# Optimization experiments

Measured on AMD Instinct MI355X. Metric: run time of the kernel, lower is better.

Reference implementation:

```python
import jax, jax.numpy as jnp
import numpy as np

SEQ, B, H, NP, HN = 2048, 2, 2048, 16, 128
SCALE = 1.0 / 11.313708498984761  # 1/sqrt(128), hardcoded in the source baddbmm


def setup_inputs() -> dict:
    key = jax.random.key(0)
    k1, k2, k3 = jax.random.split(key, 3)
    return {
        "hidden_states": jax.random.normal(k1, (SEQ, B, H), dtype=jnp.float32),
        "w_qkv": jax.random.normal(k2, (3 * H, H), dtype=jnp.float32) * 0.02,
        "w_out": jax.random.normal(k3, (H, H), dtype=jnp.float32) * 0.02,
    }


def reference(hidden_states, w_qkv, w_out):
    s, b, h = hidden_states.shape
    # QKV projection (column-parallel linear, no bias): [s, b, 3h]
    qkv = hidden_states @ w_qkv.T
    # [s, b, np, 3*hn] then split (num_query_groups == num_heads)
    qkv = qkv.reshape(s, b, NP, 3 * HN)
    q, k, v = qkv[..., :HN], qkv[..., HN:2 * HN], qkv[..., 2 * HN:]
    # baddbmm QK^T with alpha = 1/sqrt(128): scores [b, np, sq, sk]
    scores = jnp.einsum("sbnh,tbnh->bnst", q, k) * SCALE
    # scale_t == 1 then plain softmax (fallback path; no mask applied)
    prob = jax.nn.softmax(scores, axis=-1)
    # context: bmm(prob, V) -> [sq, b, np, hn] -> [sq, b, h]
    ctx = jnp.einsum("bnst,tbnh->sbnh", prob, v).reshape(s, b, h)
    # row-parallel output linear (no bias)
    return ctx @ w_out.T
```

## Files before the change

kernel.cpp:

```cpp
#include <hip/hip_runtime.h>
#include <stdint.h>

#define SEQ 2048
#define BATCH 2
#define HID 2048
#define NHEADS 16
#define HDIM 128
#define QKV_LD 6144
#define SCALE_F 0.08838834764831845f
#define LOG2E_F 1.4426950408889634f

typedef unsigned short u16;
using bf16x8 = __attribute__((ext_vector_type(8))) short;
using f32x4  = __attribute__((ext_vector_type(4))) float;

__device__ inline u16 f2bf(float f) {
  union { float f; uint32_t u; } c; c.f = f;
  uint32_t u = c.u;
  uint32_t r = (u + 0x7fffu + ((u >> 16) & 1u)) >> 16;
  return (u16)r;
}

__device__ inline void gl_lds16(const u16* g, u16* l) {
  __builtin_amdgcn_global_load_lds((const __attribute__((address_space(1))) void*)g,
                                   (__attribute__((address_space(3))) void*)l,
                                   16, 0, 0);
}

__global__ void cvt_all(const float* __restrict__ hs, const float* __restrict__ wqkv,
                        const float* __restrict__ wout, u16* __restrict__ ws_out) {
  int i = blockIdx.x * blockDim.x + threadIdx.x;
  const float* src;
  int j;
  float sc = 1.0f;
  if (i < 2097152) { src = hs; j = i; }
  else if (i < 5242880) {
    j = i - 2097152; src = wqkv;
    const int f = j >> 9;
    if ((f % 384) < 128) sc = SCALE_F;
  } else { j = i - 5242880; src = wout; }
  float4 v = ((const float4*)src)[j];
  ushort4 o;
  o.x = f2bf(v.x * sc); o.y = f2bf(v.y * sc); o.z = f2bf(v.z * sc); o.w = f2bf(v.w * sc);
  ((ushort4*)ws_out)[i] = o;
}

template<bool OUT_BF16>
__global__ __launch_bounds__(256)
void gemm_bt(const u16* __restrict__ A, const u16* __restrict__ Bw,
             void* __restrict__ Cout, int M, int N, int K) {
  __shared__ __align__(16) u16 As[128 * 64];
  __shared__ __align__(16) u16 Bs[128 * 64];
  const int bm = blockIdx.x, bn = blockIdx.y;
  const int tid = threadIdx.x;
  const int wave = tid >> 6, lane = tid & 63;
  const int quad = lane >> 4, l16 = lane & 15;
  const int wm = (wave >> 1) * 64, wn = (wave & 1) * 64;
  f32x4 acc[4][4] = {};

  const u16* Ablk = A + (size_t)(bm * 128) * K;
  const u16* Bblk = Bw + (size_t)(bn * 128) * K;

  for (int k0 = 0; k0 < K; k0 += 64) {
    __syncthreads();
    #pragma unroll
    for (int p = 0; p < 4; ++p) {
      int j = p * 256 + tid;
      int r = j >> 3, cs = j & 7, c = cs ^ (r & 7);
      gl_lds16(Ablk + (size_t)r * K + k0 + c * 8, As + (p * 256 + wave * 64) * 8);
      gl_lds16(Bblk + (size_t)r * K + k0 + c * 8, Bs + (p * 256 + wave * 64) * 8);
    }
    __syncthreads();
    #pragma unroll
    for (int ks = 0; ks < 2; ++ks) {
      bf16x8 af[4], bfr[4];
      #pragma unroll
      for (int mt = 0; mt < 4; ++mt) {
        int row = wm + mt * 16 + l16;
        int cc = (ks * 4 + quad) ^ (row & 7);
        af[mt] = *(const bf16x8*)&As[(row * 8 + cc) * 8];
      }
      #pragma unroll
      for (int nt = 0; nt < 4; ++nt) {
        int row = wn + nt * 16 + l16;
        int cc = (ks * 4 + quad) ^ (row & 7);
        bfr[nt] = *(const bf16x8*)&Bs[(row * 8 + cc) * 8];
      }
      #pragma unroll
      for (int mt = 0; mt < 4; ++mt)
        #pragma unroll
        for (int nt = 0; nt < 4; ++nt)
          acc[mt][nt] = __builtin_amdgcn_mfma_f32_16x16x32_bf16(af[mt], bfr[nt], acc[mt][nt], 0, 0, 0);
    }
  }

  #pragma unroll
  for (int mt = 0; mt < 4; ++mt) {
    #pragma unroll
    for (int nt = 0; nt < 4; ++nt) {
      #pragma unroll
      for (int r = 0; r < 4; ++r) {
        int row = bm * 128 + wm + mt * 16 + quad * 4 + r;
        int col = bn * 128 + wn + nt * 16 + l16;
        float v = acc[mt][nt][r];
        if (OUT_BF16) ((u16*)Cout)[(size_t)row * N + col] = f2bf(v);
        else          ((float*)Cout)[(size_t)row * N + col] = v;
      }
    }
  }
}

__global__ __launch_bounds__(256)
void transpose_v(const u16* __restrict__ qkv, u16* __restrict__ vt) {
  __shared__ u16 Vs[64][132];
  const int st = blockIdx.x, head = blockIdx.y, b = blockIdx.z;
  const int s0 = st * 64;
  const int t = threadIdx.x;
  {
    const int r = t >> 2, c0 = (t & 3) * 32;
    const u16* src = qkv + ((size_t)(s0 + r) * BATCH + b) * QKV_LD + head * 384 + 256 + c0;
    #pragma unroll
    for (int j = 0; j < 4; ++j)
      *(uint4*)&Vs[r][c0 + j * 8] = *(const uint4*)(src + j * 8);
  }
  __syncthreads();
  {
    const int hd = t & 127, sc = (t >> 7) * 32;
    u16 tmp[32];
    #pragma unroll
    for (int j = 0; j < 32; ++j) tmp[j] = Vs[sc + j][hd];
    u16* dst = vt + ((size_t)(b * NHEADS + head) * HDIM + hd) * SEQ + s0 + sc;
    #pragma unroll
    for (int j = 0; j < 4; ++j)
      *(uint4*)&dst[j * 8] = *(const uint4*)&tmp[j * 8];
  }
}

__global__ __launch_bounds__(512, 2)
void attn(const u16* __restrict__ qkv, const u16* __restrict__ vt_g, u16* __restrict__ ctx) {
  const int qt = blockIdx.x, head = blockIdx.y, b = blockIdx.z;
  const int q0 = qt * 256;
  __shared__ __align__(16) u16 Ks[64 * 128];
  __shared__ __align__(16) u16 Vt[144 * 64];
  __shared__ __align__(16) u16 Ps[256 * 72];
  const int tid = threadIdx.x;
  const int wave = tid >> 6, lane = tid & 63;
  const int quad = lane >> 4, l16 = lane & 15;

  const u16* qkv_bh = qkv + (size_t)b * QKV_LD + head * 384;
  const u16* vt = vt_g + (size_t)(b * NHEADS + head) * HDIM * SEQ;

  if (tid < 128) {
    const int row = 128 + (tid >> 3), c = tid & 7;
    const u16 v = (row == 128) ? (u16)0x3F80 : (u16)0;
    ushort4 q4; q4.x = v; q4.y = v; q4.z = v; q4.w = v;
    *(ushort4*)&Vt[(row * 8 + c) * 8] = q4;
    *(ushort4*)&Vt[(row * 8 + c) * 8 + 4] = q4;
  }

  bf16x8 qf[2][4];
  #pragma unroll
  for (int h = 0; h < 4; ++h) {
    __syncthreads();
    #pragma unroll
    for (int p = 0; p < 2; ++p) {
      int j = p * 512 + tid;
      int r = j >> 4, cs = j & 15, c = cs ^ (r & 7);
      gl_lds16(qkv_bh + (size_t)(q0 + h * 64 + r) * (BATCH * QKV_LD) + c * 8,
               Ks + (p * 512 + wave * 64) * 8);
    }
    __syncthreads();
    if ((wave >> 1) == h) {
      #pragma unroll
      for (int mt = 0; mt < 2; ++mt)
        #pragma unroll
        for (int ks = 0; ks < 4; ++ks) {
          int row = (wave & 1) * 32 + mt * 16 + l16;
          int cc = (ks * 4 + quad) ^ (row & 7);
          qf[mt][ks] = *(const bf16x8*)&Ks[(row * 16 + cc) * 8];
        }
    }
  }

  f32x4 o[2][9] = {};

  for (int kt = 0; kt < SEQ; kt += 64) {
    __syncthreads();
    #pragma unroll
    for (int p = 0; p < 2; ++p) {
      int j = p * 512 + tid;
      int r = j >> 4, cs = j & 15, c = cs ^ (r & 7);
      gl_lds16(qkv_bh + (size_t)(kt + r) * (BATCH * QKV_LD) + 128 + c * 8,
               Ks + (p * 512 + wave * 64) * 8);
    }
    #pragma unroll
    for (int p = 0; p < 2; ++p) {
      int j = p * 512 + tid;
      int hd = j >> 3, cs = j & 7, c = cs ^ (hd & 7);
      gl_lds16(vt + (size_t)hd * SEQ + kt + c * 8,
               Vt + (p * 512 + wave * 64) * 8);
    }
    __syncthreads();

    f32x4 s[2][4] = {};
    #pragma unroll
    for (int ks = 0; ks < 4; ++ks) {
      bf16x8 bk[4];
      #pragma unroll
      for (int nt = 0; nt < 4; ++nt) {
        int row = nt * 16 + l16;
        int cc = (ks * 4 + quad) ^ (row & 7);
        bk[nt] = *(const bf16x8*)&Ks[(row * 16 + cc) * 8];
      }
      #pragma unroll
      for (int mt = 0; mt < 2; ++mt)
        #pragma unroll
        for (int nt = 0; nt < 4; ++nt)
          s[mt][nt] = __builtin_amdgcn_mfma_f32_16x16x32_bf16(qf[mt][ks], bk[nt], s[mt][nt], 0, 0, 0);
    }

    #pragma unroll
    for (int mt = 0; mt < 2; ++mt)
      #pragma unroll
      for (int r = 0; r < 4; ++r) {
        const int prow = (wave * 32 + mt * 16 + quad * 4 + r) * 72;
        #pragma unroll
        for (int nt = 0; nt < 4; ++nt) {
          float ex = __builtin_amdgcn_exp2f(s[mt][nt][r] * LOG2E_F);
          union { float f; uint32_t u; } cv; cv.f = ex;
          Ps[prow + nt * 16 + l16] = (u16)(cv.u >> 16);
        }
      }

    #pragma unroll
    for (int ks = 0; ks < 2; ++ks) {
      bf16x8 ap[2], bv[9];
      #pragma unroll
      for (int mt = 0; mt < 2; ++mt)
        ap[mt] = *(const bf16x8*)&Ps[(wave * 32 + mt * 16 + l16) * 72 + ks * 32 + quad * 8];
      #pragma unroll
      for (int nt = 0; nt < 9; ++nt) {
        int hd = nt * 16 + l16;
        int cc = (ks * 4 + quad) ^ (hd & 7);
        bv[nt] = *(const bf16x8*)&Vt[(hd * 8 + cc) * 8];
      }
      #pragma unroll
      for (int mt = 0; mt < 2; ++mt)
        #pragma unroll
        for (int nt = 0; nt < 9; ++nt)
          o[mt][nt] = __builtin_amdgcn_mfma_f32_16x16x32_bf16(ap[mt], bv[nt], o[mt][nt], 0, 0, 0);
    }
  }

  #pragma unroll
  for (int mt = 0; mt < 2; ++mt)
    #pragma unroll
    for (int r = 0; r < 4; ++r) {
      const float lv = __shfl(o[mt][8][r], lane & 48);
      const float inv_l = 1.0f / lv;
      const int srow = q0 + wave * 32 + mt * 16 + quad * 4 + r;
      u16* dst = ctx + ((size_t)srow * BATCH + b) * HID + head * HDIM;
      #pragma unroll
      for (int nt = 0; nt < 8; ++nt)
        dst[nt * 16 + l16] = f2bf(o[mt][nt][r] * inv_l);
    }
}

extern "C" void kernel_launch(void* const* d_in, const int* in_sizes, int n_in,
                              void* d_out, int out_size, void* d_ws, size_t ws_size,
                              hipStream_t stream) {
  const float* hs   = (const float*)d_in[0];
  const float* wqkv = (const float*)d_in[1];
  const float* wout = (const float*)d_in[2];
  float* out = (float*)d_out;
  char* ws = (char*)d_ws;

  u16* hs_bf   = (u16*)(ws);
  u16* wqkv_bf = (u16*)(ws + 16777216);
  u16* wout_bf = (u16*)(ws + 41943040);
  u16* qkv_bf  = (u16*)(ws + 50331648);
  u16* ctx_bf  = (u16*)(ws + 100663296);
  u16* vt_bf   = hs_bf;

  cvt_all<<<24576, 256, 0, stream>>>(hs, wqkv, wout, (u16*)ws);

  gemm_bt<true><<<dim3(32, 48), 256, 0, stream>>>(hs_bf, wqkv_bf, qkv_bf, 4096, 6144, 2048);

  transpose_v<<<dim3(32, NHEADS, BATCH), 256, 0, stream>>>(qkv_bf, vt_bf);

  attn<<<dim3(8, NHEADS, BATCH), 512, 0, stream>>>(qkv_bf, vt_bf, ctx_bf);

  gemm_bt<false><<<dim3(32, 16), 256, 0, stream>>>(ctx_bf, wout_bf, out, 4096, 2048, 2048);
}
```

Baseline: 386.2 us.

## Fuse V transpose into QKV GEMM epilogue and transpose attention MFMA layout

The QKV GEMM now writes V tiles directly in transposed [b,head,hd,seq] layout from its epilogue, which removes the separate transpose_v kernel and its extra read and write of V. The attention kernel computes S^T = K·Q^T and O^T = V^T·P^T, so each lane holds four consecutive keys or head dims. That allows vectorized ushort4 writes of P into a swizzled, unpadded LDS buffer and vectorized ctx stores. Costs include uncoalesced 4-byte scattered global writes for V in the GEMM epilogue, and workspace buffers are reassigned so ctx reuses the hidden-states buffer.

```diff
diff --git a/kernel.cpp b/kernel.cpp
--- a/kernel.cpp
+++ b/kernel.cpp
@@ -45,10 +45,10 @@
   ((ushort4*)ws_out)[i] = o;
 }
 
-template<bool OUT_BF16>
+template<int MODE>
 __global__ __launch_bounds__(256)
 void gemm_bt(const u16* __restrict__ A, const u16* __restrict__ Bw,
-             void* __restrict__ Cout, int M, int N, int K) {
+             void* __restrict__ Cout, u16* __restrict__ vt, int M, int N, int K) {
   __shared__ __align__(16) u16 As[128 * 64];
   __shared__ __align__(16) u16 Bs[128 * 64];
   const int bm = blockIdx.x, bn = blockIdx.y;
@@ -94,46 +94,36 @@
     }
   }
 
+  if (MODE == 1 && (bn % 3) == 2) {
+    const int h = bn / 3;
+    u16* vt0 = vt + ((size_t)h * HDIM) * SEQ;
+    u16* vt1 = vt + ((size_t)(NHEADS + h) * HDIM) * SEQ;
+    #pragma unroll
+    for (int mt = 0; mt < 4; ++mt)
+      #pragma unroll
+      for (int nt = 0; nt < 4; ++nt) {
+        const int hd = wn + nt * 16 + l16;
+        const int s0 = (bm * 128 + wm + mt * 16 + quad * 4) >> 1;
+        uint32_t w0 = (uint32_t)f2bf(acc[mt][nt][0]) | ((uint32_t)f2bf(acc[mt][nt][2]) << 16);
+        uint32_t w1 = (uint32_t)f2bf(acc[mt][nt][1]) | ((uint32_t)f2bf(acc[mt][nt][3]) << 16);
+        *(uint32_t*)&vt0[(size_t)hd * SEQ + s0] = w0;
+        *(uint32_t*)&vt1[(size_t)hd * SEQ + s0] = w1;
+      }
+    return;
+  }
+
   #pragma unroll
-  for (int mt = 0; mt < 4; ++mt) {
-    #pragma unroll
-    for (int nt = 0; nt < 4; ++nt) {
+  for (int mt = 0; mt < 4; ++mt)
+    #pragma unroll
+    for (int nt = 0; nt < 4; ++nt)
       #pragma unroll
       for (int r = 0; r < 4; ++r) {
         int row = bm * 128 + wm + mt * 16 + quad * 4 + r;
         int col = bn * 128 + wn + nt * 16 + l16;
         float v = acc[mt][nt][r];
-        if (OUT_BF16) ((u16*)Cout)[(size_t)row * N + col] = f2bf(v);
-        else          ((float*)Cout)[(size_t)row * N + col] = v;
-      }
-    }
-  }
-}
-
-__global__ __launch_bounds__(256)
-void transpose_v(const u16* __restrict__ qkv, u16* __restrict__ vt) {
-  __shared__ u16 Vs[64][132];
-  const int st = blockIdx.x, head = blockIdx.y, b = blockIdx.z;
-  const int s0 = st * 64;
-  const int t = threadIdx.x;
-  {
-    const int r = t >> 2, c0 = (t & 3) * 32;
-    const u16* src = qkv + ((size_t)(s0 + r) * BATCH + b) * QKV_LD + head * 384 + 256 + c0;
-    #pragma unroll
-    for (int j = 0; j < 4; ++j)
-      *(uint4*)&Vs[r][c0 + j * 8] = *(const uint4*)(src + j * 8);
-  }
-  __syncthreads();
-  {
-    const int hd = t & 127, sc = (t >> 7) * 32;
-    u16 tmp[32];
-    #pragma unroll
-    for (int j = 0; j < 32; ++j) tmp[j] = Vs[sc + j][hd];
-    u16* dst = vt + ((size_t)(b * NHEADS + head) * HDIM + hd) * SEQ + s0 + sc;
-    #pragma unroll
-    for (int j = 0; j < 4; ++j)
-      *(uint4*)&dst[j * 8] = *(const uint4*)&tmp[j * 8];
-  }
+        if (MODE == 1) ((u16*)Cout)[(size_t)row * N + col] = f2bf(v);
+        else           ((float*)Cout)[(size_t)row * N + col] = v;
+      }
 }
 
 __global__ __launch_bounds__(512, 2)
@@ -142,7 +132,7 @@
   const int q0 = qt * 256;
   __shared__ __align__(16) u16 Ks[64 * 128];
   __shared__ __align__(16) u16 Vt[144 * 64];
-  __shared__ __align__(16) u16 Ps[256 * 72];
+  __shared__ __align__(16) u16 PsT[256 * 64];
   const int tid = threadIdx.x;
   const int wave = tid >> 6, lane = tid & 63;
   const int quad = lane >> 4, l16 = lane & 15;
@@ -172,17 +162,17 @@
     __syncthreads();
     if ((wave >> 1) == h) {
       #pragma unroll
-      for (int mt = 0; mt < 2; ++mt)
+      for (int nt = 0; nt < 2; ++nt)
         #pragma unroll
         for (int ks = 0; ks < 4; ++ks) {
-          int row = (wave & 1) * 32 + mt * 16 + l16;
+          int row = (wave & 1) * 32 + nt * 16 + l16;
           int cc = (ks * 4 + quad) ^ (row & 7);
-          qf[mt][ks] = *(const bf16x8*)&Ks[(row * 16 + cc) * 8];
+          qf[nt][ks] = *(const bf16x8*)&Ks[(row * 16 + cc) * 8];
         }
     }
   }
 
-  f32x4 o[2][9] = {};
+  f32x4 ot[9][2] = {};
 
   for (int kt = 0; kt < SEQ; kt += 64) {
     __syncthreads();
@@ -202,68 +192,77 @@
     }
     __syncthreads();
 
-    f32x4 s[2][4] = {};
+    f32x4 st[4][2] = {};
     #pragma unroll
     for (int ks = 0; ks < 4; ++ks) {
-      bf16x8 bk[4];
-      #pragma unroll
-      for (int nt = 0; nt < 4; ++nt) {
-        int row = nt * 16 + l16;
-        int cc = (ks * 4 + quad) ^ (row & 7);
-        bk[nt] = *(const bf16x8*)&Ks[(row * 16 + cc) * 8];
-      }
-      #pragma unroll
-      for (int mt = 0; mt < 2; ++mt)
-        #pragma unroll
-        for (int nt = 0; nt < 4; ++nt)
-          s[mt][nt] = __builtin_amdgcn_mfma_f32_16x16x32_bf16(qf[mt][ks], bk[nt], s[mt][nt], 0, 0, 0);
-    }
-
-    #pragma unroll
-    for (int mt = 0; mt < 2; ++mt)
-      #pragma unroll
-      for (int r = 0; r < 4; ++r) {
-        const int prow = (wave * 32 + mt * 16 + quad * 4 + r) * 72;
-        #pragma unroll
-        for (int nt = 0; nt < 4; ++nt) {
-          float ex = __builtin_amdgcn_exp2f(s[mt][nt][r] * LOG2E_F);
-          union { float f; uint32_t u; } cv; cv.f = ex;
-          Ps[prow + nt * 16 + l16] = (u16)(cv.u >> 16);
-        }
+      bf16x8 kf[4];
+      #pragma unroll
+      for (int mt = 0; mt < 4; ++mt) {
+        int key = mt * 16 + l16;
+        int cc = (ks * 4 + quad) ^ (key & 7);
+        kf[mt] = *(const bf16x8*)&Ks[(key * 16 + cc) * 8];
+      }
+      #pragma unroll
+      for (int mt = 0; mt < 4; ++mt)
+        #pragma unroll
+        for (int nt = 0; nt < 2; ++nt)
+          st[mt][nt] = __builtin_amdgcn_mfma_f32_16x16x32_bf16(kf[mt], qf[nt][ks], st[mt][nt], 0, 0, 0);
+    }
+
+    #pragma unroll
+    for (int mt = 0; mt < 4; ++mt)
+      #pragma unroll
+      for (int nt = 0; nt < 2; ++nt) {
+        ushort4 pk;
+        union { float f; uint32_t u; } cv;
+        cv.f = __builtin_amdgcn_exp2f(st[mt][nt][0] * LOG2E_F); pk.x = (u16)(cv.u >> 16);
+        cv.f = __builtin_amdgcn_exp2f(st[mt][nt][1] * LOG2E_F); pk.y = (u16)(cv.u >> 16);
+        cv.f = __builtin_amdgcn_exp2f(st[mt][nt][2] * LOG2E_F); pk.z = (u16)(cv.u >> 16);
+        cv.f = __builtin_amdgcn_exp2f(st[mt][nt][3] * LOG2E_F); pk.w = (u16)(cv.u >> 16);
+        const int q = wave * 32 + nt * 16 + l16;
+        const int kc = mt * 2 + (quad >> 1);
+        *(ushort4*)&PsT[q * 64 + ((kc ^ (l16 & 7)) * 8 + (quad & 1) * 4)] = pk;
       }
 
     #pragma unroll
     for (int ks = 0; ks < 2; ++ks) {
-      bf16x8 ap[2], bv[9];
-      #pragma unroll
-      for (int mt = 0; mt < 2; ++mt)
-        ap[mt] = *(const bf16x8*)&Ps[(wave * 32 + mt * 16 + l16) * 72 + ks * 32 + quad * 8];
-      #pragma unroll
-      for (int nt = 0; nt < 9; ++nt) {
-        int hd = nt * 16 + l16;
-        int cc = (ks * 4 + quad) ^ (hd & 7);
-        bv[nt] = *(const bf16x8*)&Vt[(hd * 8 + cc) * 8];
-      }
-      #pragma unroll
-      for (int mt = 0; mt < 2; ++mt)
-        #pragma unroll
-        for (int nt = 0; nt < 9; ++nt)
-          o[mt][nt] = __builtin_amdgcn_mfma_f32_16x16x32_bf16(ap[mt], bv[nt], o[mt][nt], 0, 0, 0);
+      bf16x8 pf[2], vf[9];
+      #pragma unroll
+      for (int nt = 0; nt < 2; ++nt) {
+        const int q = wave * 32 + nt * 16 + l16;
+        const int cc = (ks * 4 + quad) ^ (l16 & 7);
+        pf[nt] = *(const bf16x8*)&PsT[q * 64 + cc * 8];
+      }
+      #pragma unroll
+      for (int mt = 0; mt < 9; ++mt) {
+        const int hd = mt * 16 + l16;
+        const int cc = (ks * 4 + quad) ^ (hd & 7);
+        vf[mt] = *(const bf16x8*)&Vt[(hd * 8 + cc) * 8];
+      }
+      #pragma unroll
+      for (int mt = 0; mt < 9; ++mt)
+        #pragma unroll
+        for (int nt = 0; nt < 2; ++nt)
+          ot[mt][nt] = __builtin_amdgcn_mfma_f32_16x16x32_bf16(vf[mt], pf[nt], ot[mt][nt], 0, 0, 0);
     }
   }
 
   #pragma unroll
-  for (int mt = 0; mt < 2; ++mt)
-    #pragma unroll
-    for (int r = 0; r < 4; ++r) {
-      const float lv = __shfl(o[mt][8][r], lane & 48);
-      const float inv_l = 1.0f / lv;
-      const int srow = q0 + wave * 32 + mt * 16 + quad * 4 + r;
-      u16* dst = ctx + ((size_t)srow * BATCH + b) * HID + head * HDIM;
-      #pragma unroll
-      for (int nt = 0; nt < 8; ++nt)
-        dst[nt * 16 + l16] = f2bf(o[mt][nt][r] * inv_l);
-    }
+  for (int nt = 0; nt < 2; ++nt) {
+    const float lv = __shfl(ot[8][nt][0], l16);
+    const float inv_l = 1.0f / lv;
+    const int s = q0 + wave * 32 + nt * 16 + l16;
+    u16* dst = ctx + ((size_t)s * BATCH + b) * HID + head * HDIM;
+    #pragma unroll
+    for (int mt = 0; mt < 8; ++mt) {
+      ushort4 w;
+      w.x = f2bf(ot[mt][nt][0] * inv_l);
+      w.y = f2bf(ot[mt][nt][1] * inv_l);
+      w.z = f2bf(ot[mt][nt][2] * inv_l);
+      w.w = f2bf(ot[mt][nt][3] * inv_l);
+      *(ushort4*)&dst[mt * 16 + quad * 4] = w;
+    }
+  }
 }
 
 extern "C" void kernel_launch(void* const* d_in, const int* in_sizes, int n_in,
@@ -279,16 +278,14 @@
   u16* wqkv_bf = (u16*)(ws + 16777216);
   u16* wout_bf = (u16*)(ws + 41943040);
   u16* qkv_bf  = (u16*)(ws + 50331648);
-  u16* ctx_bf  = (u16*)(ws + 100663296);
-  u16* vt_bf   = hs_bf;
+  u16* vt_bf   = (u16*)(ws + 100663296);
+  u16* ctx_bf  = hs_bf;
 
   cvt_all<<<24576, 256, 0, stream>>>(hs, wqkv, wout, (u16*)ws);
 
-  gemm_bt<true><<<dim3(32, 48), 256, 0, stream>>>(hs_bf, wqkv_bf, qkv_bf, 4096, 6144, 2048);
-
-  transpose_v<<<dim3(32, NHEADS, BATCH), 256, 0, stream>>>(qkv_bf, vt_bf);
+  gemm_bt<1><<<dim3(32, 48), 256, 0, stream>>>(hs_bf, wqkv_bf, qkv_bf, vt_bf, 4096, 6144, 2048);
 
   attn<<<dim3(8, NHEADS, BATCH), 512, 0, stream>>>(qkv_bf, vt_bf, ctx_bf);
 
-  gemm_bt<false><<<dim3(32, 16), 256, 0, stream>>>(ctx_bf, wout_bf, out, 4096, 2048, 2048);
-}
+  gemm_bt<0><<<dim3(32, 16), 256, 0, stream>>>(ctx_bf, wout_bf, out, nullptr, 4096, 2048, 2048);
+}
```

Result: faster. 373.1 us (-3.4%).
